# Performance work log

Hardware: AMD Instinct MI355X
Metric: run time of the kernel (lower is better)

Reference implementation:

```python
import jax, jax.numpy as jnp
import numpy as np

N_NODES = 100000
N_CLASSES = 16


def _graph_conv(x, W, b, src, dst, n_nodes):
    # DGL GraphConv norm='both': D_out^{-1/2} on src, aggregate, D_in^{-1/2} on dst.
    ones = jnp.ones(src.shape[0], x.dtype)
    deg_out = jnp.clip(jax.ops.segment_sum(ones, src, num_segments=n_nodes), 1.0)
    deg_in = jnp.clip(jax.ops.segment_sum(ones, dst, num_segments=n_nodes), 1.0)
    h = (x * jax.lax.rsqrt(deg_out)[:, None]) @ W          # [N, out] project first (in>=out)
    agg = jax.ops.segment_sum(h[src], dst, num_segments=n_nodes)  # gather-scatter
    return agg * jax.lax.rsqrt(deg_in)[:, None] + b


def _hetero_conv(x, W, b, edge_src, edge_dst, n_nodes):
    # HeteroGraphConv(aggregate='sum') over R relations, each its own GraphConv.
    out = _graph_conv(x, W[0], b[0], edge_src[0], edge_dst[0], n_nodes)
    for r in range(1, W.shape[0]):
        out = out + _graph_conv(x, W[r], b[r], edge_src[r], edge_dst[r], n_nodes)
    return out


def reference(x, W0, b0, W_mu, b_mu, W_ls, b_ls, edge_src, edge_dst,
              pos_src, pos_dst, neg_src, neg_dst):
    n = x.shape[0]
    h1 = jax.nn.relu(_hetero_conv(x, W0, b0, edge_src, edge_dst, n))
    mean = _hetero_conv(h1, W_mu, b_mu, edge_src, edge_dst, n)
    log_std = _hetero_conv(h1, W_ls, b_ls, edge_src, edge_dst, n)
    noise = jax.random.normal(jax.random.key(42), mean.shape, mean.dtype)
    h = mean + noise * jnp.exp(log_std)                     # VGAE reparameterization
    pos_score = jnp.sum(h[pos_src] * h[pos_dst], axis=-1, keepdims=True)  # u_dot_v
    neg_score = jnp.sum(h[neg_src] * h[neg_dst], axis=-1, keepdims=True)
    return pos_score, neg_score, h


def setup_inputs() -> dict:
    key = jax.random.key(0)
    ks = jax.random.split(key, 12)
    R, E, EP = 3, 1600000, 500000
    in_f, hid, out = 128, 64, N_CLASSES
    return {
        "x": jax.random.normal(ks[0], (N_NODES, in_f), jnp.float32),
        "W0": jax.random.normal(ks[1], (R, in_f, hid), jnp.float32) * (1.0 / np.sqrt(in_f)),
        "b0": jnp.zeros((R, hid), jnp.float32),
        "W_mu": jax.random.normal(ks[2], (R, hid, out), jnp.float32) * (1.0 / np.sqrt(hid)),
        "b_mu": jnp.zeros((R, out), jnp.float32),
        "W_ls": jax.random.normal(ks[3], (R, hid, out), jnp.float32) * (1.0 / np.sqrt(hid)),
        "b_ls": jnp.zeros((R, out), jnp.float32),
        "edge_src": jax.random.randint(ks[4], (R, E), 0, N_NODES, jnp.int32),
        "edge_dst": jax.random.randint(ks[5], (R, E), 0, N_NODES, jnp.int32),
        "pos_src": jax.random.randint(ks[6], (EP,), 0, N_NODES, jnp.int32),
        "pos_dst": jax.random.randint(ks[7], (EP,), 0, N_NODES, jnp.int32),
        "neg_src": jax.random.randint(ks[8], (EP,), 0, N_NODES, jnp.int32),
        "neg_dst": jax.random.randint(ks[9], (EP,), 0, N_NODES, jnp.int32),
    }
```

## Files before the change

### kernel.cpp

```cpp
#include <hip/hip_runtime.h>
#include <math.h>

#define N_NODES 100000
#define NREL 3
#define E_PER 1600000
#define E_TOT 4800000
#define EP 500000
#define F_IN 128
#define F_HID 64
#define F_OUT 16
#define NRN 300000

#define NSEG 7
#define SEGSZ 16000
#define NBLK 32
#define CHUNK (E_PER / NBLK)

#define OFF_DOUT    0
#define OFF_DINVIN  300000
#define OFF_CNT     600000
#define OFF_G       900000
#define OFF_BSUM    1200000
#define OFF_CSR     1201024
#define OFF_ESLOT   6001024
#define OFF_HPROJ   6001024
#define OFF_H1      12401088
#define OFF_L2      18801088
#define WS_NEED_CSR 22001088
#define ODINV_OUT 0
#define ODINV_IN  300000
#define OH1ACC    600000
#define OHPROJ    7000000
#define OL2ACC    13400000

__device__ __forceinline__ float atomAddF(float* p, float v) {
    return unsafeAtomicAdd(p, v);
}

__device__ __forceinline__ unsigned rotl32(unsigned x, unsigned d) {
    return (x << d) | (x >> (32u - d));
}

__device__ float jax_noise(unsigned i) {
    const unsigned ks0 = 0u, ks1 = 42u;
    const unsigned ks2 = ks0 ^ ks1 ^ 0x1BD11BDAu;
    unsigned x0 = 0u + ks0;
    unsigned x1 = i + ks1;
#define TFR(r) { x0 += x1; x1 = rotl32(x1, r); x1 ^= x0; }
    TFR(13) TFR(15) TFR(26) TFR(6)
    x0 += ks1; x1 += ks2 + 1u;
    TFR(17) TFR(29) TFR(16) TFR(24)
    x0 += ks2; x1 += ks0 + 2u;
    TFR(13) TFR(15) TFR(26) TFR(6)
    x0 += ks0; x1 += ks1 + 3u;
    TFR(17) TFR(29) TFR(16) TFR(24)
    x0 += ks1; x1 += ks2 + 4u;
    TFR(13) TFR(15) TFR(26) TFR(6)
    x0 += ks2; x1 += ks0 + 5u;
#undef TFR
    const unsigned bits = x0 ^ x1;
    float f = __uint_as_float((bits >> 9) | 0x3f800000u) - 1.0f;
    const float lo = -0.99999994f;
    float u = fmaxf(lo, f * 2.0f + lo);
    float w = -log1pf(-u * u);
    float p;
    if (w < 5.0f) {
        w -= 2.5f;
        p = 2.81022636e-08f;
        p = fmaf(p, w, 3.43273939e-07f);
        p = fmaf(p, w, -3.5233877e-06f);
        p = fmaf(p, w, -4.39150654e-06f);
        p = fmaf(p, w, 0.00021858087f);
        p = fmaf(p, w, -0.00125372503f);
        p = fmaf(p, w, -0.00417768164f);
        p = fmaf(p, w, 0.246640727f);
        p = fmaf(p, w, 1.50140941f);
    } else {
        w = sqrtf(w) - 3.0f;
        p = -0.000200214257f;
        p = fmaf(p, w, 0.000100950558f);
        p = fmaf(p, w, 0.00134934322f);
        p = fmaf(p, w, -0.00367342844f);
        p = fmaf(p, w, 0.00573950773f);
        p = fmaf(p, w, -0.0076224613f);
        p = fmaf(p, w, 0.00943887047f);
        p = fmaf(p, w, 1.00167406f);
        p = fmaf(p, w, 2.83297682f);
    }
    return 1.41421356237f * (p * u);
}

__global__ __launch_bounds__(512) void k_histin(const int* __restrict__ ed,
                                                int* __restrict__ cnt,
                                                int* __restrict__ eslot) {
    __shared__ int lds[SEGSZ];
    const int r = blockIdx.z, g = blockIdx.y, b = blockIdx.x;
    const int lo = g * SEGSZ;
    const int hi = min(lo + SEGSZ, N_NODES);
    const int nbins = hi - lo;
    for (int i = threadIdx.x; i < nbins; i += 512) lds[i] = 0;
    __syncthreads();
    const int e0 = r * E_PER + b * CHUNK;
    const int e1 = e0 + CHUNK;
    for (int e = e0 + threadIdx.x * 4; e + 4 <= e1; e += 512 * 4) {
        const int4 d4 = *(const int4*)(ed + e);
        if (d4.x >= lo && d4.x < hi) atomicAdd(&lds[d4.x - lo], 1);
        if (d4.y >= lo && d4.y < hi) atomicAdd(&lds[d4.y - lo], 1);
        if (d4.z >= lo && d4.z < hi) atomicAdd(&lds[d4.z - lo], 1);
        if (d4.w >= lo && d4.w < hi) atomicAdd(&lds[d4.w - lo], 1);
    }
    __syncthreads();
    for (int i = threadIdx.x; i < nbins; i += 512) {
        const int c = lds[i];
        lds[i] = c ? atomicAdd(&cnt[r * N_NODES + lo + i], c) : 0;
    }
    __syncthreads();
    for (int e = e0 + threadIdx.x * 4; e + 4 <= e1; e += 512 * 4) {
        const int4 d4 = *(const int4*)(ed + e);
        if (d4.x >= lo && d4.x < hi) eslot[e]     = atomicAdd(&lds[d4.x - lo], 1);
        if (d4.y >= lo && d4.y < hi) eslot[e + 1] = atomicAdd(&lds[d4.y - lo], 1);
        if (d4.z >= lo && d4.z < hi) eslot[e + 2] = atomicAdd(&lds[d4.z - lo], 1);
        if (d4.w >= lo && d4.w < hi) eslot[e + 3] = atomicAdd(&lds[d4.w - lo], 1);
    }
}

__global__ __launch_bounds__(512) void k_histout(const int* __restrict__ es,
                                                 int* __restrict__ dout) {
    __shared__ int lds[SEGSZ];
    const int r = blockIdx.z, g = blockIdx.y, b = blockIdx.x;
    const int lo = g * SEGSZ;
    const int hi = min(lo + SEGSZ, N_NODES);
    const int nbins = hi - lo;
    for (int i = threadIdx.x; i < nbins; i += 512) lds[i] = 0;
    __syncthreads();
    const int e0 = r * E_PER + b * CHUNK;
    const int e1 = e0 + CHUNK;
    for (int e = e0 + threadIdx.x * 4; e + 4 <= e1; e += 512 * 4) {
        const int4 s4 = *(const int4*)(es + e);
        if (s4.x >= lo && s4.x < hi) atomicAdd(&lds[s4.x - lo], 1);
        if (s4.y >= lo && s4.y < hi) atomicAdd(&lds[s4.y - lo], 1);
        if (s4.z >= lo && s4.z < hi) atomicAdd(&lds[s4.z - lo], 1);
        if (s4.w >= lo && s4.w < hi) atomicAdd(&lds[s4.w - lo], 1);
    }
    __syncthreads();
    for (int i = threadIdx.x; i < nbins; i += 512) {
        const int c = lds[i];
        if (c) atomicAdd(&dout[r * N_NODES + lo + i], c);
    }
}

__global__ __launch_bounds__(256) void k_scanA(const int* __restrict__ cnt,
                                               int* __restrict__ bsum) {
    __shared__ int red[256];
    const int base = blockIdx.x * 1024 + threadIdx.x * 4;
    int s = 0;
#pragma unroll
    for (int q = 0; q < 4; ++q) {
        const int i = base + q;
        s += (i < NRN) ? cnt[i] : 0;
    }
    red[threadIdx.x] = s;
    __syncthreads();
    for (int w = 128; w > 0; w >>= 1) {
        if (threadIdx.x < w) red[threadIdx.x] += red[threadIdx.x + w];
        __syncthreads();
    }
    if (threadIdx.x == 0) bsum[blockIdx.x] = red[0];
}

__global__ __launch_bounds__(512) void k_scanB(int* __restrict__ bsum) {
    __shared__ int sc[512];
    const int t = threadIdx.x;
    sc[t] = (t < 294) ? bsum[t] : 0;
    __syncthreads();
    for (int o = 1; o < 512; o <<= 1) {
        const int v = (t >= o) ? sc[t - o] : 0;
        __syncthreads();
        sc[t] += v;
        __syncthreads();
    }
    bsum[t] = (t > 0) ? sc[t - 1] : 0;
}

__global__ __launch_bounds__(256) void k_scanC(const int* __restrict__ cnt,
                                               const int* __restrict__ bsum,
                                               int* __restrict__ G,
                                               float* __restrict__ dinv_in,
                                               int* doutc) {
    __shared__ int sc[256];
    const int t = threadIdx.x;
    const int base = blockIdx.x * 1024 + t * 4;
    int v[4];
    int ts = 0;
#pragma unroll
    for (int q = 0; q < 4; ++q) {
        const int i = base + q;
        v[q] = (i < NRN) ? cnt[i] : 0;
        ts += v[q];
    }
    sc[t] = ts;
    __syncthreads();
    for (int o = 1; o < 256; o <<= 1) {
        const int x = (t >= o) ? sc[t - o] : 0;
        __syncthreads();
        sc[t] += x;
        __syncthreads();
    }
    int run = bsum[blockIdx.x] + ((t > 0) ? sc[t - 1] : 0);
#pragma unroll
    for (int q = 0; q < 4; ++q) {
        const int i = base + q;
        if (i < NRN) {
            G[i] = run;
            dinv_in[i] = rsqrtf((float)max(v[q], 1));
            const int oc = doutc[i];
            ((float*)doutc)[i] = rsqrtf((float)max(oc, 1));
        }
        run += v[q];
    }
}

__global__ __launch_bounds__(256) void k_fill(const int* __restrict__ es,
                                              const int* __restrict__ ed,
                                              const int* __restrict__ eslot,
                                              const int* __restrict__ G,
                                              int* __restrict__ csr) {
    const int r = blockIdx.y;
    const int e = (blockIdx.x * 256 + threadIdx.x) * 4;
    if (e + 4 > E_PER) return;
    const int gid = r * E_PER + e;
    const int4 s4 = *(const int4*)(es + gid);
    const int4 d4 = *(const int4*)(ed + gid);
    const int4 l4 = *(const int4*)(eslot + gid);
    const int rb = r * N_NODES;
    csr[G[rb + d4.x] + l4.x] = s4.x;
    csr[G[rb + d4.y] + l4.y] = s4.y;
    csr[G[rb + d4.z] + l4.z] = s4.z;
    csr[G[rb + d4.w] + l4.w] = s4.w;
}

__global__ __launch_bounds__(256) void k_gather1(const float* __restrict__ hp,
                                                 const int* __restrict__ csr,
                                                 const int* __restrict__ G,
                                                 const float* __restrict__ dinv,
                                                 float* __restrict__ h1,
                                                 int rbase, int first) {
    const int node = (blockIdx.x * 256 + threadIdx.x) >> 6;
    const int lane = threadIdx.x & 63;
    const int l16 = lane & 15;
    const int e4 = lane >> 4;
    const int idx = rbase + node;
    const int off0 = G[idx];
    const int off1 = (idx == NRN - 1) ? E_TOT : G[idx + 1];
    float ax = 0.f, ay = 0.f, az = 0.f, aw = 0.f;
    for (int base = off0; base < off1; base += 64) {
        int m = off1 - base;
        if (m > 64) m = 64;
        const int sv = (lane < m) ? csr[base + lane] : N_NODES;
        const int nq = (m + 3) >> 2;
        for (int q = 0; q < nq; ++q) {
            const int ei = q * 4 + e4;
            const int s = __shfl(sv, ei);
            const float4 v = *(const float4*)(hp + (size_t)s * F_HID + l16 * 4);
            ax += v.x;
            ay += v.y;
            az += v.z;
            aw += v.w;
        }
    }
    ax += __shfl_xor(ax, 16); ay += __shfl_xor(ay, 16);
    az += __shfl_xor(az, 16); aw += __shfl_xor(aw, 16);
    ax += __shfl_xor(ax, 32); ay += __shfl_xor(ay, 32);
    az += __shfl_xor(az, 32); aw += __shfl_xor(aw, 32);
    if (lane < 16) {
        const float dv = dinv[idx];
        float4* dst = (float4*)(h1 + (size_t)node * F_HID) + l16;
        float4 o;
        if (first) {
            o.x = dv * ax; o.y = dv * ay; o.z = dv * az; o.w = dv * aw;
        } else {
            const float4 pr = *dst;
            o.x = pr.x + dv * ax; o.y = pr.y + dv * ay;
            o.z = pr.z + dv * az; o.w = pr.w + dv * aw;
        }
        *dst = o;
    }
}

__global__ __launch_bounds__(256) void k_gather2(const float* __restrict__ hp,
                                                 const int* __restrict__ csr,
                                                 const int* __restrict__ G,
                                                 const float* __restrict__ dinv,
                                                 float* __restrict__ l2,
                                                 int rbase, int first) {
    const int node = (blockIdx.x * 256 + threadIdx.x) >> 6;
    const int lane = threadIdx.x & 63;
    const int l8 = lane & 7;
    const int e8 = lane >> 3;
    const int idx = rbase + node;
    const int off0 = G[idx];
    const int off1 = (idx == NRN - 1) ? E_TOT : G[idx + 1];
    float ax = 0.f, ay = 0.f, az = 0.f, aw = 0.f;
    for (int base = off0; base < off1; base += 64) {
        int m = off1 - base;
        if (m > 64) m = 64;
        const int sv = (lane < m) ? csr[base + lane] : N_NODES;
        const int nq = (m + 7) >> 3;
        for (int q = 0; q < nq; ++q) {
            const int ei = q * 8 + e8;
            const int s = __shfl(sv, ei);
            const float4 v = *(const float4*)(hp + (size_t)s * 32 + l8 * 4);
            ax += v.x;
            ay += v.y;
            az += v.z;
            aw += v.w;
        }
    }
    ax += __shfl_xor(ax, 8);  ay += __shfl_xor(ay, 8);
    az += __shfl_xor(az, 8);  aw += __shfl_xor(aw, 8);
    ax += __shfl_xor(ax, 16); ay += __shfl_xor(ay, 16);
    az += __shfl_xor(az, 16); aw += __shfl_xor(aw, 16);
    ax += __shfl_xor(ax, 32); ay += __shfl_xor(ay, 32);
    az += __shfl_xor(az, 32); aw += __shfl_xor(aw, 32);
    if (lane < 8) {
        const float dv = dinv[idx];
        float4* dst = (float4*)(l2 + (size_t)node * 32) + l8;
        float4 o;
        if (first) {
            o.x = dv * ax; o.y = dv * ay; o.z = dv * az; o.w = dv * aw;
        } else {
            const float4 pr = *dst;
            o.x = pr.x + dv * ax; o.y = pr.y + dv * ay;
            o.z = pr.z + dv * az; o.w = pr.w + dv * aw;
        }
        *dst = o;
    }
}

__global__ __launch_bounds__(256) void k_gather2_fin(const float* __restrict__ hp,
                                                     const int* __restrict__ csr,
                                                     const int* __restrict__ G,
                                                     const float* __restrict__ dinv,
                                                     const float* __restrict__ l2,
                                                     const float* __restrict__ bmu,
                                                     const float* __restrict__ bls,
                                                     float* __restrict__ outh,
                                                     int rbase) {
    const int node = (blockIdx.x * 256 + threadIdx.x) >> 6;
    const int lane = threadIdx.x & 63;
    const int l8 = lane & 7;
    const int e8 = lane >> 3;
    const int idx = rbase + node;
    const int off0 = G[idx];
    const int off1 = (idx == NRN - 1) ? E_TOT : G[idx + 1];
    float ax = 0.f, ay = 0.f, az = 0.f, aw = 0.f;
    for (int base = off0; base < off1; base += 64) {
        int m = off1 - base;
        if (m > 64) m = 64;
        const int sv = (lane < m) ? csr[base + lane] : N_NODES;
        const int nq = (m + 7) >> 3;
        for (int q = 0; q < nq; ++q) {
            const int ei = q * 8 + e8;
            const int s = __shfl(sv, ei);
            const float4 v = *(const float4*)(hp + (size_t)s * 32 + l8 * 4);
            ax += v.x;
            ay += v.y;
            az += v.z;
            aw += v.w;
        }
    }
    ax += __shfl_xor(ax, 8);  ay += __shfl_xor(ay, 8);
    az += __shfl_xor(az, 8);  aw += __shfl_xor(aw, 8);
    ax += __shfl_xor(ax, 16); ay += __shfl_xor(ay, 16);
    az += __shfl_xor(az, 16); aw += __shfl_xor(aw, 16);
    ax += __shfl_xor(ax, 32); ay += __shfl_xor(ay, 32);
    az += __shfl_xor(az, 32); aw += __shfl_xor(aw, 32);
    const float dv = dinv[idx];
    const float4 pr = *((const float4*)(l2 + (size_t)node * 32) + l8);
    const float vx = pr.x + dv * ax;
    const float vy = pr.y + dv * ay;
    const float vz = pr.z + dv * az;
    const float vw = pr.w + dv * aw;
    const int srcM = lane >> 2;
    const int srcL = 4 + (lane >> 2);
    const float m0 = __shfl(vx, srcM), m1 = __shfl(vy, srcM),
                m2 = __shfl(vz, srcM), m3 = __shfl(vw, srcM);
    const float s0 = __shfl(vx, srcL), s1 = __shfl(vy, srcL),
                s2 = __shfl(vz, srcL), s3 = __shfl(vw, srcL);
    if (lane < 16) {
        const int c = lane;
        const float mm = (c & 2) ? ((c & 1) ? m3 : m2) : ((c & 1) ? m1 : m0);
        const float ss = (c & 2) ? ((c & 1) ? s3 : s2) : ((c & 1) ? s1 : s0);
        const float mean = mm + bmu[c] + bmu[16 + c] + bmu[32 + c];
        const float lstd = ss + bls[c] + bls[16 + c] + bls[32 + c];
        outh[(size_t)node * 16 + c] =
            mean + jax_noise((unsigned)(node * 16 + c)) * expf(lstd);
    }
}

__global__ __launch_bounds__(256) void k_project1(const float* __restrict__ x,
                                                  const float* __restrict__ W,
                                                  const float* __restrict__ dinv,
                                                  float* __restrict__ out) {
    __shared__ float ws[F_IN * F_HID];
    for (int i = threadIdx.x; i < F_IN * F_HID; i += 256) ws[i] = W[i];
    __syncthreads();
    for (int t = blockIdx.x * 256 + threadIdx.x; t < (N_NODES + 1) * 16;
         t += gridDim.x * 256) {
        const int n = t >> 4;
        const int c0 = (t & 15) << 2;
        const int nn = min(n, N_NODES - 1);
        const float4* xr = (const float4*)(x + (size_t)nn * F_IN);
        float a0 = 0.f, a1 = 0.f, a2 = 0.f, a3 = 0.f;
#pragma unroll 8
        for (int k4 = 0; k4 < F_IN / 4; ++k4) {
            const float4 xv = xr[k4];
            const float4 w0 = *(const float4*)(ws + (k4 * 4 + 0) * F_HID + c0);
            const float4 w1 = *(const float4*)(ws + (k4 * 4 + 1) * F_HID + c0);
            const float4 w2 = *(const float4*)(ws + (k4 * 4 + 2) * F_HID + c0);
            const float4 w3 = *(const float4*)(ws + (k4 * 4 + 3) * F_HID + c0);
            a0 = fmaf(xv.x, w0.x, a0); a1 = fmaf(xv.x, w0.y, a1);
            a2 = fmaf(xv.x, w0.z, a2); a3 = fmaf(xv.x, w0.w, a3);
            a0 = fmaf(xv.y, w1.x, a0); a1 = fmaf(xv.y, w1.y, a1);
            a2 = fmaf(xv.y, w1.z, a2); a3 = fmaf(xv.y, w1.w, a3);
            a0 = fmaf(xv.z, w2.x, a0); a1 = fmaf(xv.z, w2.y, a1);
            a2 = fmaf(xv.z, w2.z, a2); a3 = fmaf(xv.z, w2.w, a3);
            a0 = fmaf(xv.w, w3.x, a0); a1 = fmaf(xv.w, w3.y, a1);
            a2 = fmaf(xv.w, w3.z, a2); a3 = fmaf(xv.w, w3.w, a3);
        }
        const float dv = (n < N_NODES) ? dinv[nn] : 0.f;
        float4 o;
        o.x = a0 * dv; o.y = a1 * dv; o.z = a2 * dv; o.w = a3 * dv;
        *(float4*)(out + (size_t)n * F_HID + c0) = o;
    }
}

__global__ __launch_bounds__(256) void k_project2(const float* __restrict__ h1,
                                                  const float* __restrict__ b0,
                                                  const float* __restrict__ Wmu,
                                                  const float* __restrict__ Wls,
                                                  const float* __restrict__ dinv,
                                                  float* __restrict__ out) {
    __shared__ float ws[F_HID * 32];
    __shared__ float bs[F_HID];
    for (int i = threadIdx.x; i < F_HID * 32; i += 256) {
        const int k = i >> 5, c = i & 31;
        ws[i] = (c < 16) ? Wmu[k * 16 + c] : Wls[k * 16 + (c - 16)];
    }
    if (threadIdx.x < F_HID)
        bs[threadIdx.x] = b0[threadIdx.x] + b0[64 + threadIdx.x] + b0[128 + threadIdx.x];
    __syncthreads();
    for (int t = blockIdx.x * 256 + threadIdx.x; t < (N_NODES + 1) * 8;
         t += gridDim.x * 256) {
        const int n = t >> 3;
        const int c0 = (t & 7) << 2;
        const int nn = min(n, N_NODES - 1);
        const float4* hr = (const float4*)(h1 + (size_t)nn * F_HID);
        float a0 = 0.f, a1 = 0.f, a2 = 0.f, a3 = 0.f;
#pragma unroll 4
        for (int k4 = 0; k4 < F_HID / 4; ++k4) {
            const float4 hv = hr[k4];
            const float4 bv = *(const float4*)(bs + k4 * 4);
            const float r0 = fmaxf(hv.x + bv.x, 0.f);
            const float r1 = fmaxf(hv.y + bv.y, 0.f);
            const float r2 = fmaxf(hv.z + bv.z, 0.f);
            const float r3 = fmaxf(hv.w + bv.w, 0.f);
            const float4 w0 = *(const float4*)(ws + (k4 * 4 + 0) * 32 + c0);
            const float4 w1 = *(const float4*)(ws + (k4 * 4 + 1) * 32 + c0);
            const float4 w2 = *(const float4*)(ws + (k4 * 4 + 2) * 32 + c0);
            const float4 w3 = *(const float4*)(ws + (k4 * 4 + 3) * 32 + c0);
            a0 = fmaf(r0, w0.x, a0); a1 = fmaf(r0, w0.y, a1);
            a2 = fmaf(r0, w0.z, a2); a3 = fmaf(r0, w0.w, a3);
            a0 = fmaf(r1, w1.x, a0); a1 = fmaf(r1, w1.y, a1);
            a2 = fmaf(r1, w1.z, a2); a3 = fmaf(r1, w1.w, a3);
            a0 = fmaf(r2, w2.x, a0); a1 = fmaf(r2, w2.y, a1);
            a2 = fmaf(r2, w2.z, a2); a3 = fmaf(r2, w2.w, a3);
            a0 = fmaf(r3, w3.x, a0); a1 = fmaf(r3, w3.y, a1);
            a2 = fmaf(r3, w3.z, a2); a3 = fmaf(r3, w3.w, a3);
        }
        const float dv = (n < N_NODES) ? dinv[nn] : 0.f;
        float4 o;
        o.x = a0 * dv; o.y = a1 * dv; o.z = a2 * dv; o.w = a3 * dv;
        *(float4*)(out + (size_t)n * 32 + c0) = o;
    }
}

__global__ __launch_bounds__(256) void k_scores(const int* __restrict__ ps,
                                                const int* __restrict__ pd,
                                                const int* __restrict__ ns,
                                                const int* __restrict__ nd,
                                                const float* __restrict__ h,
                                                float* __restrict__ out) {
    const int i = blockIdx.x * 256 + threadIdx.x;
    if (i >= 2 * EP) return;
    const int j = (i < EP) ? i : i - EP;
    const int a = (i < EP) ? ps[j] : ns[j];
    const int b = (i < EP) ? pd[j] : nd[j];
    const float4* ha = (const float4*)(h + (size_t)a * 16);
    const float4* hb = (const float4*)(h + (size_t)b * 16);
    float s = 0.f;
#pragma unroll
    for (int q = 0; q < 4; ++q) {
        const float4 u = ha[q];
        const float4 v = hb[q];
        s += u.x * v.x + u.y * v.y + u.z * v.z + u.w * v.w;
    }
    out[i] = s;
}

__global__ __launch_bounds__(256) void k_degrees(const int* __restrict__ es,
                                                 const int* __restrict__ ed,
                                                 float* __restrict__ dout,
                                                 float* __restrict__ din) {
    const int r = blockIdx.y;
    const int e = blockIdx.x * 256 + threadIdx.x;
    const int s = es[r * E_PER + e];
    const int d = ed[r * E_PER + e];
    atomAddF(&dout[r * N_NODES + s], 1.0f);
    atomAddF(&din[r * N_NODES + d], 1.0f);
}

__global__ __launch_bounds__(256) void k_finalize_deg(float* __restrict__ d) {
    const int i = blockIdx.x * 256 + threadIdx.x;
    if (i < 2 * NRN) d[i] = 1.0f / sqrtf(fmaxf(d[i], 1.0f));
}

__global__ __launch_bounds__(256) void k_scatter1(const float* __restrict__ hp,
                                                  const int* __restrict__ es,
                                                  const int* __restrict__ ed,
                                                  const float* __restrict__ din,
                                                  float* __restrict__ acc) {
    const int t = blockIdx.x * 256 + threadIdx.x;
    const int e = t >> 6;
    const int lane = t & 63;
    const int s = es[e];
    const int d = ed[e];
    const float v = hp[s * F_HID + lane] * din[d];
    atomAddF(&acc[d * F_HID + lane], v);
}

__global__ __launch_bounds__(256) void k_scatter2(const float* __restrict__ hp,
                                                  const int* __restrict__ es,
                                                  const int* __restrict__ ed,
                                                  const float* __restrict__ din,
                                                  float* __restrict__ acc) {
    const int t = blockIdx.x * 256 + threadIdx.x;
    const int e = t >> 5;
    const int c = t & 31;
    const int s = es[e];
    const int d = ed[e];
    const float v = hp[s * 32 + c] * din[d];
    atomAddF(&acc[d * 32 + c], v);
}

__global__ __launch_bounds__(256) void k_finalize(const float* __restrict__ l2,
                                                  const float* __restrict__ bmu,
                                                  const float* __restrict__ bls,
                                                  float* __restrict__ outh) {
    const int i = blockIdx.x * 256 + threadIdx.x;
    const int n = i >> 4, c = i & 15;
    const float mean = l2[n * 32 + c] + bmu[c] + bmu[16 + c] + bmu[32 + c];
    const float lstd = l2[n * 32 + 16 + c] + bls[c] + bls[16 + c] + bls[32 + c];
    const float z = jax_noise((unsigned)i);
    outh[i] = mean + z * expf(lstd);
}

extern "C" void kernel_launch(void* const* d_in, const int* in_sizes, int n_in,
                              void* d_out, int out_size, void* d_ws, size_t ws_size,
                              hipStream_t stream) {
    const float* x   = (const float*)d_in[0];
    const float* W0  = (const float*)d_in[1];
    const float* b0  = (const float*)d_in[2];
    const float* Wmu = (const float*)d_in[3];
    const float* bmu = (const float*)d_in[4];
    const float* Wls = (const float*)d_in[5];
    const float* bls = (const float*)d_in[6];
    const int* es = (const int*)d_in[7];
    const int* ed = (const int*)d_in[8];
    const int* ps = (const int*)d_in[9];
    const int* pd = (const int*)d_in[10];
    const int* ns = (const int*)d_in[11];
    const int* nd = (const int*)d_in[12];
    float* out = (float*)d_out;
    float* wsf = (float*)d_ws;

    if (ws_size >= (size_t)WS_NEED_CSR * sizeof(float)) {
        int*   doutc   = (int*)(wsf + OFF_DOUT);
        float* doutf   = wsf + OFF_DOUT;
        float* dinv_in = wsf + OFF_DINVIN;
        int*   cnt     = (int*)(wsf + OFF_CNT);
        int*   G       = (int*)(wsf + OFF_G);
        int*   bsum    = (int*)(wsf + OFF_BSUM);
        int*   csr     = (int*)(wsf + OFF_CSR);
        int*   eslot   = (int*)(wsf + OFF_ESLOT);
        float* hproj   = wsf + OFF_HPROJ;
        float* h1acc   = wsf + OFF_H1;
        float* l2acc   = wsf + OFF_L2;

        hipMemsetAsync(doutc, 0, (size_t)NRN * sizeof(int), stream);
        hipMemsetAsync(cnt, 0, (size_t)NRN * sizeof(int), stream);

        k_histin<<<dim3(NBLK, NSEG, NREL), 512, 0, stream>>>(ed, cnt, eslot);
        k_histout<<<dim3(NBLK, NSEG, NREL), 512, 0, stream>>>(es, doutc);
        k_scanA<<<294, 256, 0, stream>>>(cnt, bsum);
        k_scanB<<<1, 512, 0, stream>>>(bsum);
        k_scanC<<<294, 256, 0, stream>>>(cnt, bsum, G, dinv_in, doutc);
        k_fill<<<dim3((E_PER / 4 + 255) / 256, NREL), 256, 0, stream>>>(
            es, ed, eslot, G, csr);

        for (int r = 0; r < NREL; ++r) {
            k_project1<<<1280, 256, 0, stream>>>(
                x, W0 + (size_t)r * F_IN * F_HID, doutf + (size_t)r * N_NODES, hproj);
            k_gather1<<<N_NODES / 4, 256, 0, stream>>>(
                hproj, csr, G, dinv_in, h1acc, r * N_NODES, r == 0);
        }
        for (int r = 0; r < NREL; ++r) {
            k_project2<<<1024, 256, 0, stream>>>(
                h1acc, b0, Wmu + (size_t)r * F_HID * F_OUT,
                Wls + (size_t)r * F_HID * F_OUT, doutf + (size_t)r * N_NODES, hproj);
            if (r < NREL - 1) {
                k_gather2<<<N_NODES / 4, 256, 0, stream>>>(
                    hproj, csr, G, dinv_in, l2acc, r * N_NODES, r == 0);
            } else {
                k_gather2_fin<<<N_NODES / 4, 256, 0, stream>>>(
                    hproj, csr, G, dinv_in, l2acc, bmu, bls, out + 2 * EP,
                    r * N_NODES);
            }
        }
        k_scores<<<(2 * EP + 255) / 256, 256, 0, stream>>>(
            ps, pd, ns, nd, out + 2 * EP, out);
    } else {
        float* dinv_out = wsf + ODINV_OUT;
        float* dinv_in  = wsf + ODINV_IN;
        float* h1acc    = wsf + OH1ACC;
        float* hproj    = wsf + OHPROJ;
        float* l2acc    = wsf + OL2ACC;

        hipMemsetAsync(dinv_out, 0, (size_t)2 * NRN * sizeof(float), stream);
        hipMemsetAsync(h1acc, 0, (size_t)N_NODES * F_HID * sizeof(float), stream);
        hipMemsetAsync(l2acc, 0, (size_t)N_NODES * 32 * sizeof(float), stream);

        k_degrees<<<dim3(E_PER / 256, NREL), 256, 0, stream>>>(es, ed, dinv_out, dinv_in);
        k_finalize_deg<<<(2 * NRN + 255) / 256, 256, 0, stream>>>(wsf);

        for (int r = 0; r < NREL; ++r) {
            k_project1<<<1280, 256, 0, stream>>>(
                x, W0 + (size_t)r * F_IN * F_HID, dinv_out + (size_t)r * N_NODES, hproj);
            k_scatter1<<<E_PER / 4, 256, 0, stream>>>(
                hproj, es + (size_t)r * E_PER, ed + (size_t)r * E_PER,
                dinv_in + (size_t)r * N_NODES, h1acc);
        }
        for (int r = 0; r < NREL; ++r) {
            k_project2<<<1024, 256, 0, stream>>>(
                h1acc, b0, Wmu + (size_t)r * F_HID * F_OUT,
                Wls + (size_t)r * F_HID * F_OUT, dinv_out + (size_t)r * N_NODES, hproj);
            k_scatter2<<<E_PER / 8, 256, 0, stream>>>(
                hproj, es + (size_t)r * E_PER, ed + (size_t)r * E_PER,
                dinv_in + (size_t)r * N_NODES, l2acc);
        }
        k_finalize<<<N_NODES * F_OUT / 256, 256, 0, stream>>>(
            l2acc, bmu, bls, out + 2 * EP);
        k_scores<<<(2 * EP + 255) / 256, 256, 0, stream>>>(
            ps, pd, ns, nd, out + 2 * EP, out);
    }
}
```

Baseline: 860.2 us.

## Replace segmented LDS histograms with global atomics and atomic-decrement CSR fill

The two segmented LDS-histogram kernels, which each reread the edge lists once per node segment, become a single kernel that does direct global atomic increments on the in- and out-degree counters. The per-edge slot array is gone: the CSR fill kernel now claims slots by atomically decrementing the count array. This cuts redundant edge-list passes and the slot-array traffic, but puts all counting contention on global atomics and makes the order of neighbours within a CSR row nondeterministic.

After: 1.297 ms. 50.8% more time.

```diff
diff --git a/kernel.cpp b/kernel.cpp
--- a/kernel.cpp
+++ b/kernel.cpp
@@ -11,18 +11,12 @@
 #define F_OUT 16
 #define NRN 300000
 
-#define NSEG 7
-#define SEGSZ 16000
-#define NBLK 32
-#define CHUNK (E_PER / NBLK)
-
 #define OFF_DOUT    0
 #define OFF_DINVIN  300000
 #define OFF_CNT     600000
 #define OFF_G       900000
 #define OFF_BSUM    1200000
 #define OFF_CSR     1201024
-#define OFF_ESLOT   6001024
 #define OFF_HPROJ   6001024
 #define OFF_H1      12401088
 #define OFF_L2      18801088
@@ -90,63 +84,35 @@
     return 1.41421356237f * (p * u);
 }
 
-__global__ __launch_bounds__(512) void k_histin(const int* __restrict__ ed,
-                                                int* __restrict__ cnt,
-                                                int* __restrict__ eslot) {
-    __shared__ int lds[SEGSZ];
-    const int r = blockIdx.z, g = blockIdx.y, b = blockIdx.x;
-    const int lo = g * SEGSZ;
-    const int hi = min(lo + SEGSZ, N_NODES);
-    const int nbins = hi - lo;
-    for (int i = threadIdx.x; i < nbins; i += 512) lds[i] = 0;
-    __syncthreads();
-    const int e0 = r * E_PER + b * CHUNK;
-    const int e1 = e0 + CHUNK;
-    for (int e = e0 + threadIdx.x * 4; e + 4 <= e1; e += 512 * 4) {
-        const int4 d4 = *(const int4*)(ed + e);
-        if (d4.x >= lo && d4.x < hi) atomicAdd(&lds[d4.x - lo], 1);
-        if (d4.y >= lo && d4.y < hi) atomicAdd(&lds[d4.y - lo], 1);
-        if (d4.z >= lo && d4.z < hi) atomicAdd(&lds[d4.z - lo], 1);
-        if (d4.w >= lo && d4.w < hi) atomicAdd(&lds[d4.w - lo], 1);
-    }
-    __syncthreads();
-    for (int i = threadIdx.x; i < nbins; i += 512) {
-        const int c = lds[i];
-        lds[i] = c ? atomicAdd(&cnt[r * N_NODES + lo + i], c) : 0;
-    }
-    __syncthreads();
-    for (int e = e0 + threadIdx.x * 4; e + 4 <= e1; e += 512 * 4) {
-        const int4 d4 = *(const int4*)(ed + e);
-        if (d4.x >= lo && d4.x < hi) eslot[e]     = atomicAdd(&lds[d4.x - lo], 1);
-        if (d4.y >= lo && d4.y < hi) eslot[e + 1] = atomicAdd(&lds[d4.y - lo], 1);
-        if (d4.z >= lo && d4.z < hi) eslot[e + 2] = atomicAdd(&lds[d4.z - lo], 1);
-        if (d4.w >= lo && d4.w < hi) eslot[e + 3] = atomicAdd(&lds[d4.w - lo], 1);
-    }
-}
-
-__global__ __launch_bounds__(512) void k_histout(const int* __restrict__ es,
-                                                 int* __restrict__ dout) {
-    __shared__ int lds[SEGSZ];
-    const int r = blockIdx.z, g = blockIdx.y, b = blockIdx.x;
-    const int lo = g * SEGSZ;
-    const int hi = min(lo + SEGSZ, N_NODES);
-    const int nbins = hi - lo;
-    for (int i = threadIdx.x; i < nbins; i += 512) lds[i] = 0;
-    __syncthreads();
-    const int e0 = r * E_PER + b * CHUNK;
-    const int e1 = e0 + CHUNK;
-    for (int e = e0 + threadIdx.x * 4; e + 4 <= e1; e += 512 * 4) {
-        const int4 s4 = *(const int4*)(es + e);
-        if (s4.x >= lo && s4.x < hi) atomicAdd(&lds[s4.x - lo], 1);
-        if (s4.y >= lo && s4.y < hi) atomicAdd(&lds[s4.y - lo], 1);
-        if (s4.z >= lo && s4.z < hi) atomicAdd(&lds[s4.z - lo], 1);
-        if (s4.w >= lo && s4.w < hi) atomicAdd(&lds[s4.w - lo], 1);
-    }
-    __syncthreads();
-    for (int i = threadIdx.x; i < nbins; i += 512) {
-        const int c = lds[i];
-        if (c) atomicAdd(&dout[r * N_NODES + lo + i], c);
-    }
+__global__ __launch_bounds__(256) void k_hist(const int* __restrict__ es,
+                                              const int* __restrict__ ed,
+                                              int* __restrict__ dout,
+                                              int* __restrict__ cnt) {
+    const int r = blockIdx.y;
+    const int e = (blockIdx.x * 256 + threadIdx.x) * 8;
+    if (e + 8 > E_PER) return;
+    const int gid = r * E_PER + e;
+    const int rb = r * N_NODES;
+    const int4 sa = *(const int4*)(es + gid);
+    const int4 sb = *(const int4*)(es + gid + 4);
+    const int4 da = *(const int4*)(ed + gid);
+    const int4 db = *(const int4*)(ed + gid + 4);
+    atomicAdd(&dout[rb + sa.x], 1);
+    atomicAdd(&dout[rb + sa.y], 1);
+    atomicAdd(&dout[rb + sa.z], 1);
+    atomicAdd(&dout[rb + sa.w], 1);
+    atomicAdd(&dout[rb + sb.x], 1);
+    atomicAdd(&dout[rb + sb.y], 1);
+    atomicAdd(&dout[rb + sb.z], 1);
+    atomicAdd(&dout[rb + sb.w], 1);
+    atomicAdd(&cnt[rb + da.x], 1);
+    atomicAdd(&cnt[rb + da.y], 1);
+    atomicAdd(&cnt[rb + da.z], 1);
+    atomicAdd(&cnt[rb + da.w], 1);
+    atomicAdd(&cnt[rb + db.x], 1);
+    atomicAdd(&cnt[rb + db.y], 1);
+    atomicAdd(&cnt[rb + db.z], 1);
+    atomicAdd(&cnt[rb + db.w], 1);
 }
 
 __global__ __launch_bounds__(256) void k_scanA(const int* __restrict__ cnt,
@@ -220,23 +186,38 @@
     }
 }
 
-__global__ __launch_bounds__(256) void k_fill(const int* __restrict__ es,
-                                              const int* __restrict__ ed,
-                                              const int* __restrict__ eslot,
-                                              const int* __restrict__ G,
-                                              int* __restrict__ csr) {
+__global__ __launch_bounds__(256) void k_filld(const int* __restrict__ es,
+                                               const int* __restrict__ ed,
+                                               int* __restrict__ cnt,
+                                               const int* __restrict__ G,
+                                               int* __restrict__ csr) {
     const int r = blockIdx.y;
     const int e = (blockIdx.x * 256 + threadIdx.x) * 4;
     if (e + 4 > E_PER) return;
     const int gid = r * E_PER + e;
     const int4 s4 = *(const int4*)(es + gid);
     const int4 d4 = *(const int4*)(ed + gid);
-    const int4 l4 = *(const int4*)(eslot + gid);
     const int rb = r * N_NODES;
-    csr[G[rb + d4.x] + l4.x] = s4.x;
-    csr[G[rb + d4.y] + l4.y] = s4.y;
-    csr[G[rb + d4.z] + l4.z] = s4.z;
-    csr[G[rb + d4.w] + l4.w] = s4.w;
+    {
+        const int i = rb + d4.x;
+        const int sl = atomicAdd(&cnt[i], -1) - 1;
+        csr[G[i] + sl] = s4.x;
+    }
+    {
+        const int i = rb + d4.y;
+        const int sl = atomicAdd(&cnt[i], -1) - 1;
+        csr[G[i] + sl] = s4.y;
+    }
+    {
+        const int i = rb + d4.z;
+        const int sl = atomicAdd(&cnt[i], -1) - 1;
+        csr[G[i] + sl] = s4.z;
+    }
+    {
+        const int i = rb + d4.w;
+        const int sl = atomicAdd(&cnt[i], -1) - 1;
+        csr[G[i] + sl] = s4.w;
+    }
 }
 
 __global__ __launch_bounds__(256) void k_gather1(const float* __restrict__ hp,
@@ -592,7 +573,6 @@
         int*   G       = (int*)(wsf + OFF_G);
         int*   bsum    = (int*)(wsf + OFF_BSUM);
         int*   csr     = (int*)(wsf + OFF_CSR);
-        int*   eslot   = (int*)(wsf + OFF_ESLOT);
         float* hproj   = wsf + OFF_HPROJ;
         float* h1acc   = wsf + OFF_H1;
         float* l2acc   = wsf + OFF_L2;
@@ -600,13 +580,13 @@
         hipMemsetAsync(doutc, 0, (size_t)NRN * sizeof(int), stream);
         hipMemsetAsync(cnt, 0, (size_t)NRN * sizeof(int), stream);
 
-        k_histin<<<dim3(NBLK, NSEG, NREL), 512, 0, stream>>>(ed, cnt, eslot);
-        k_histout<<<dim3(NBLK, NSEG, NREL), 512, 0, stream>>>(es, doutc);
+        k_hist<<<dim3((E_PER / 8 + 255) / 256, NREL), 256, 0, stream>>>(
+            es, ed, doutc, cnt);
         k_scanA<<<294, 256, 0, stream>>>(cnt, bsum);
         k_scanB<<<1, 512, 0, stream>>>(bsum);
         k_scanC<<<294, 256, 0, stream>>>(cnt, bsum, G, dinv_in, doutc);
-        k_fill<<<dim3((E_PER / 4 + 255) / 256, NREL), 256, 0, stream>>>(
-            es, ed, eslot, G, csr);
+        k_filld<<<dim3((E_PER / 4 + 255) / 256, NREL), 256, 0, stream>>>(
+            es, ed, cnt, G, csr);
 
         for (int r = 0; r < NREL; ++r) {
             k_project1<<<1280, 256, 0, stream>>>(
```

## Fuse layer-2 gathers across relations and pack out-degree histogram into 16-bit bins

Applied to the files above, without the earlier changes.

The three per-relation layer-2 gather kernels become one kernel. It reads three separate projection buffers and accumulates all relations in registers, so the l2 accumulator read-modify-write round trips and two launches go away. The out-degree histogram now packs two 16-bit counters per LDS word, which allows larger segments (4 instead of 7) and fewer passes over the edge list. The risks are overflow of a 16-bit counter if any node gets 65536 or more edges in one chunk, and a larger workspace because the projections must be kept side by side.

After: 859.8 us. No clear change (-0.0%).

```diff
diff --git a/kernel.cpp b/kernel.cpp
--- a/kernel.cpp
+++ b/kernel.cpp
@@ -15,6 +15,8 @@
 #define SEGSZ 16000
 #define NBLK 32
 #define CHUNK (E_PER / NBLK)
+#define SEGO 25000
+#define NSEGO 4
 
 #define OFF_DOUT    0
 #define OFF_DINVIN  300000
@@ -25,8 +27,9 @@
 #define OFF_ESLOT   6001024
 #define OFF_HPROJ   6001024
 #define OFF_H1      12401088
-#define OFF_L2      18801088
-#define WS_NEED_CSR 22001088
+#define OFF_HP22    18801088
+#define WS_NEED_CSR 22001120
+#define HP2SZ 3200032
 #define ODINV_OUT 0
 #define ODINV_IN  300000
 #define OH1ACC    600000
@@ -126,26 +129,40 @@
 
 __global__ __launch_bounds__(512) void k_histout(const int* __restrict__ es,
                                                  int* __restrict__ dout) {
-    __shared__ int lds[SEGSZ];
+    __shared__ int lds[SEGO / 2];
     const int r = blockIdx.z, g = blockIdx.y, b = blockIdx.x;
-    const int lo = g * SEGSZ;
-    const int hi = min(lo + SEGSZ, N_NODES);
-    const int nbins = hi - lo;
-    for (int i = threadIdx.x; i < nbins; i += 512) lds[i] = 0;
+    const int lo = g * SEGO;
+    const int hi = lo + SEGO;
+    for (int i = threadIdx.x; i < SEGO / 2; i += 512) lds[i] = 0;
     __syncthreads();
     const int e0 = r * E_PER + b * CHUNK;
     const int e1 = e0 + CHUNK;
     for (int e = e0 + threadIdx.x * 4; e + 4 <= e1; e += 512 * 4) {
         const int4 s4 = *(const int4*)(es + e);
-        if (s4.x >= lo && s4.x < hi) atomicAdd(&lds[s4.x - lo], 1);
-        if (s4.y >= lo && s4.y < hi) atomicAdd(&lds[s4.y - lo], 1);
-        if (s4.z >= lo && s4.z < hi) atomicAdd(&lds[s4.z - lo], 1);
-        if (s4.w >= lo && s4.w < hi) atomicAdd(&lds[s4.w - lo], 1);
-    }
-    __syncthreads();
-    for (int i = threadIdx.x; i < nbins; i += 512) {
-        const int c = lds[i];
-        if (c) atomicAdd(&dout[r * N_NODES + lo + i], c);
+        if (s4.x >= lo && s4.x < hi) {
+            const int i = s4.x - lo;
+            atomicAdd(&lds[i >> 1], 1 << ((i & 1) * 16));
+        }
+        if (s4.y >= lo && s4.y < hi) {
+            const int i = s4.y - lo;
+            atomicAdd(&lds[i >> 1], 1 << ((i & 1) * 16));
+        }
+        if (s4.z >= lo && s4.z < hi) {
+            const int i = s4.z - lo;
+            atomicAdd(&lds[i >> 1], 1 << ((i & 1) * 16));
+        }
+        if (s4.w >= lo && s4.w < hi) {
+            const int i = s4.w - lo;
+            atomicAdd(&lds[i >> 1], 1 << ((i & 1) * 16));
+        }
+    }
+    __syncthreads();
+    for (int i = threadIdx.x; i < SEGO / 2; i += 512) {
+        const unsigned c = (unsigned)lds[i];
+        const int c0 = (int)(c & 0xffffu);
+        const int c1 = (int)(c >> 16);
+        if (c0) atomicAdd(&dout[r * N_NODES + lo + 2 * i], c0);
+        if (c1) atomicAdd(&dout[r * N_NODES + lo + 2 * i + 1], c1);
     }
 }
 
@@ -287,106 +304,60 @@
     }
 }
 
-__global__ __launch_bounds__(256) void k_gather2(const float* __restrict__ hp,
-                                                 const int* __restrict__ csr,
-                                                 const int* __restrict__ G,
-                                                 const float* __restrict__ dinv,
-                                                 float* __restrict__ l2,
-                                                 int rbase, int first) {
+__global__ __launch_bounds__(256) void k_gather2_all(const float* __restrict__ hp0,
+                                                     const float* __restrict__ hp1,
+                                                     const float* __restrict__ hp2,
+                                                     const int* __restrict__ csr,
+                                                     const int* __restrict__ G,
+                                                     const float* __restrict__ dinv,
+                                                     const float* __restrict__ bmu,
+                                                     const float* __restrict__ bls,
+                                                     float* __restrict__ outh) {
     const int node = (blockIdx.x * 256 + threadIdx.x) >> 6;
     const int lane = threadIdx.x & 63;
     const int l8 = lane & 7;
     const int e8 = lane >> 3;
-    const int idx = rbase + node;
-    const int off0 = G[idx];
-    const int off1 = (idx == NRN - 1) ? E_TOT : G[idx + 1];
-    float ax = 0.f, ay = 0.f, az = 0.f, aw = 0.f;
-    for (int base = off0; base < off1; base += 64) {
-        int m = off1 - base;
-        if (m > 64) m = 64;
-        const int sv = (lane < m) ? csr[base + lane] : N_NODES;
-        const int nq = (m + 7) >> 3;
-        for (int q = 0; q < nq; ++q) {
-            const int ei = q * 8 + e8;
-            const int s = __shfl(sv, ei);
-            const float4 v = *(const float4*)(hp + (size_t)s * 32 + l8 * 4);
-            ax += v.x;
-            ay += v.y;
-            az += v.z;
-            aw += v.w;
-        }
-    }
-    ax += __shfl_xor(ax, 8);  ay += __shfl_xor(ay, 8);
-    az += __shfl_xor(az, 8);  aw += __shfl_xor(aw, 8);
-    ax += __shfl_xor(ax, 16); ay += __shfl_xor(ay, 16);
-    az += __shfl_xor(az, 16); aw += __shfl_xor(aw, 16);
-    ax += __shfl_xor(ax, 32); ay += __shfl_xor(ay, 32);
-    az += __shfl_xor(az, 32); aw += __shfl_xor(aw, 32);
-    if (lane < 8) {
+    float ox = 0.f, oy = 0.f, oz = 0.f, ow = 0.f;
+#pragma unroll
+    for (int r = 0; r < NREL; ++r) {
+        const float* hp = (r == 0) ? hp0 : (r == 1) ? hp1 : hp2;
+        const int idx = r * N_NODES + node;
+        const int off0 = G[idx];
+        const int off1 = (idx == NRN - 1) ? E_TOT : G[idx + 1];
+        float ax = 0.f, ay = 0.f, az = 0.f, aw = 0.f;
+        for (int base = off0; base < off1; base += 64) {
+            int m = off1 - base;
+            if (m > 64) m = 64;
+            const int sv = (lane < m) ? csr[base + lane] : N_NODES;
+            const int nq = (m + 7) >> 3;
+            for (int q = 0; q < nq; ++q) {
+                const int ei = q * 8 + e8;
+                const int s = __shfl(sv, ei);
+                const float4 v = *(const float4*)(hp + (size_t)s * 32 + l8 * 4);
+                ax += v.x;
+                ay += v.y;
+                az += v.z;
+                aw += v.w;
+            }
+        }
+        ax += __shfl_xor(ax, 8);  ay += __shfl_xor(ay, 8);
+        az += __shfl_xor(az, 8);  aw += __shfl_xor(aw, 8);
+        ax += __shfl_xor(ax, 16); ay += __shfl_xor(ay, 16);
+        az += __shfl_xor(az, 16); aw += __shfl_xor(aw, 16);
+        ax += __shfl_xor(ax, 32); ay += __shfl_xor(ay, 32);
+        az += __shfl_xor(az, 32); aw += __shfl_xor(aw, 32);
         const float dv = dinv[idx];
-        float4* dst = (float4*)(l2 + (size_t)node * 32) + l8;
-        float4 o;
-        if (first) {
-            o.x = dv * ax; o.y = dv * ay; o.z = dv * az; o.w = dv * aw;
-        } else {
-            const float4 pr = *dst;
-            o.x = pr.x + dv * ax; o.y = pr.y + dv * ay;
-            o.z = pr.z + dv * az; o.w = pr.w + dv * aw;
-        }
-        *dst = o;
-    }
-}
-
-__global__ __launch_bounds__(256) void k_gather2_fin(const float* __restrict__ hp,
-                                                     const int* __restrict__ csr,
-                                                     const int* __restrict__ G,
-                                                     const float* __restrict__ dinv,
-                                                     const float* __restrict__ l2,
-                                                     const float* __restrict__ bmu,
-                                                     const float* __restrict__ bls,
-                                                     float* __restrict__ outh,
-                                                     int rbase) {
-    const int node = (blockIdx.x * 256 + threadIdx.x) >> 6;
-    const int lane = threadIdx.x & 63;
-    const int l8 = lane & 7;
-    const int e8 = lane >> 3;
-    const int idx = rbase + node;
-    const int off0 = G[idx];
-    const int off1 = (idx == NRN - 1) ? E_TOT : G[idx + 1];
-    float ax = 0.f, ay = 0.f, az = 0.f, aw = 0.f;
-    for (int base = off0; base < off1; base += 64) {
-        int m = off1 - base;
-        if (m > 64) m = 64;
-        const int sv = (lane < m) ? csr[base + lane] : N_NODES;
-        const int nq = (m + 7) >> 3;
-        for (int q = 0; q < nq; ++q) {
-            const int ei = q * 8 + e8;
-            const int s = __shfl(sv, ei);
-            const float4 v = *(const float4*)(hp + (size_t)s * 32 + l8 * 4);
-            ax += v.x;
-            ay += v.y;
-            az += v.z;
-            aw += v.w;
-        }
-    }
-    ax += __shfl_xor(ax, 8);  ay += __shfl_xor(ay, 8);
-    az += __shfl_xor(az, 8);  aw += __shfl_xor(aw, 8);
-    ax += __shfl_xor(ax, 16); ay += __shfl_xor(ay, 16);
-    az += __shfl_xor(az, 16); aw += __shfl_xor(aw, 16);
-    ax += __shfl_xor(ax, 32); ay += __shfl_xor(ay, 32);
-    az += __shfl_xor(az, 32); aw += __shfl_xor(aw, 32);
-    const float dv = dinv[idx];
-    const float4 pr = *((const float4*)(l2 + (size_t)node * 32) + l8);
-    const float vx = pr.x + dv * ax;
-    const float vy = pr.y + dv * ay;
-    const float vz = pr.z + dv * az;
-    const float vw = pr.w + dv * aw;
+        ox = fmaf(dv, ax, ox);
+        oy = fmaf(dv, ay, oy);
+        oz = fmaf(dv, az, oz);
+        ow = fmaf(dv, aw, ow);
+    }
     const int srcM = lane >> 2;
     const int srcL = 4 + (lane >> 2);
-    const float m0 = __shfl(vx, srcM), m1 = __shfl(vy, srcM),
-                m2 = __shfl(vz, srcM), m3 = __shfl(vw, srcM);
-    const float s0 = __shfl(vx, srcL), s1 = __shfl(vy, srcL),
-                s2 = __shfl(vz, srcL), s3 = __shfl(vw, srcL);
+    const float m0 = __shfl(ox, srcM), m1 = __shfl(oy, srcM),
+                m2 = __shfl(oz, srcM), m3 = __shfl(ow, srcM);
+    const float s0 = __shfl(ox, srcL), s1 = __shfl(oy, srcL),
+                s2 = __shfl(oz, srcL), s3 = __shfl(ow, srcL);
     if (lane < 16) {
         const int c = lane;
         const float mm = (c & 2) ? ((c & 1) ? m3 : m2) : ((c & 1) ? m1 : m0);
@@ -594,14 +565,16 @@
         int*   csr     = (int*)(wsf + OFF_CSR);
         int*   eslot   = (int*)(wsf + OFF_ESLOT);
         float* hproj   = wsf + OFF_HPROJ;
+        float* hp20    = wsf + OFF_HPROJ;
+        float* hp21    = wsf + OFF_HPROJ + HP2SZ;
+        float* hp22    = wsf + OFF_HP22;
         float* h1acc   = wsf + OFF_H1;
-        float* l2acc   = wsf + OFF_L2;
 
         hipMemsetAsync(doutc, 0, (size_t)NRN * sizeof(int), stream);
         hipMemsetAsync(cnt, 0, (size_t)NRN * sizeof(int), stream);
 
         k_histin<<<dim3(NBLK, NSEG, NREL), 512, 0, stream>>>(ed, cnt, eslot);
-        k_histout<<<dim3(NBLK, NSEG, NREL), 512, 0, stream>>>(es, doutc);
+        k_histout<<<dim3(NBLK, NSEGO, NREL), 512, 0, stream>>>(es, doutc);
         k_scanA<<<294, 256, 0, stream>>>(cnt, bsum);
         k_scanB<<<1, 512, 0, stream>>>(bsum);
         k_scanC<<<294, 256, 0, stream>>>(cnt, bsum, G, dinv_in, doutc);
@@ -614,19 +587,15 @@
             k_gather1<<<N_NODES / 4, 256, 0, stream>>>(
                 hproj, csr, G, dinv_in, h1acc, r * N_NODES, r == 0);
         }
+        float* hp2s[NREL] = {hp20, hp21, hp22};
         for (int r = 0; r < NREL; ++r) {
             k_project2<<<1024, 256, 0, stream>>>(
                 h1acc, b0, Wmu + (size_t)r * F_HID * F_OUT,
-                Wls + (size_t)r * F_HID * F_OUT, doutf + (size_t)r * N_NODES, hproj);
-            if (r < NREL - 1) {
-                k_gather2<<<N_NODES / 4, 256, 0, stream>>>(
-                    hproj, csr, G, dinv_in, l2acc, r * N_NODES, r == 0);
-            } else {
-                k_gather2_fin<<<N_NODES / 4, 256, 0, stream>>>(
-                    hproj, csr, G, dinv_in, l2acc, bmu, bls, out + 2 * EP,
-                    r * N_NODES);
-            }
-        }
+                Wls + (size_t)r * F_HID * F_OUT, doutf + (size_t)r * N_NODES,
+                hp2s[r]);
+        }
+        k_gather2_all<<<N_NODES / 4, 256, 0, stream>>>(
+            hp20, hp21, hp22, csr, G, dinv_in, bmu, bls, out + 2 * EP);
         k_scores<<<(2 * EP + 255) / 256, 256, 0, stream>>>(
             ps, pd, ns, nd, out + 2 * EP, out);
     } else {
```
